# Optimization experiments

Measured on AMD Instinct MI355X. Metric: run time of the kernel, lower is better.

Reference implementation:

```python
import jax, jax.numpy as jnp
import numpy as np
from jax import lax

IN_CH = 512
OUT_CH = 512
K = 3
W_DIM = 512
PAD = K // 2
EPS = 1e-8


def setup_inputs() -> dict:
    key = jax.random.key(0)
    k1, k2, k3, k4 = jax.random.split(key, 4)
    B, H, W = 8, 64, 64
    x = jax.random.normal(k1, (B, IN_CH, H, W), dtype=jnp.float32)
    w = jax.random.normal(k2, (B, W_DIM), dtype=jnp.float32)
    weight = jax.random.normal(k3, (OUT_CH, IN_CH, K, K), dtype=jnp.float32)
    bias = jnp.zeros((OUT_CH,), dtype=jnp.float32)
    # nn.Linear(512, in_ch): weight [in_ch, 512], bias [in_ch]
    lim = 1.0 / np.sqrt(W_DIM)
    affine_w = jax.random.uniform(k4, (IN_CH, W_DIM), dtype=jnp.float32, minval=-lim, maxval=lim)
    affine_b = jnp.zeros((IN_CH,), dtype=jnp.float32)
    return {"x": x, "w": w, "weight": weight, "bias": bias,
            "affine_w": affine_w, "affine_b": affine_b}


def _conv_one(xi, wi):
    # xi: [C, H, W], wi: [O, C, K, K] -> [O, H, W]
    out = lax.conv_general_dilated(
        xi[None], wi, window_strides=(1, 1),
        padding=[(PAD, PAD), (PAD, PAD)],
        dimension_numbers=("NCHW", "OIHW", "NCHW"))
    return out[0]


def reference(x, w, weight, bias, affine_w, affine_b):
    # style: [B, C] -> broadcast as [B, 1, C, 1, 1]
    style = w @ affine_w.T + affine_b
    wmod = weight[None] * (style[:, None, :, None, None] + 1.0)  # [B, O, C, K, K]
    # demodulate
    sigma = lax.rsqrt(jnp.sum(wmod * wmod, axis=(2, 3, 4), keepdims=True) + EPS)
    wmod = wmod * sigma
    # per-sample conv (equivalent to groups=B grouped conv)
    out = jax.vmap(_conv_one)(x, wmod)  # [B, O, H, W]
    return out + bias[None, :, None, None]
```

## Files before the change

### kernel.cpp

```cpp
#include <hip/hip_runtime.h>
#include <hip/hip_bf16.h>

typedef __attribute__((ext_vector_type(8))) short bf16x8;
typedef __attribute__((ext_vector_type(4))) float f32x4;

#define FSW(c) (((c) >> 1) & 3)

static __device__ __forceinline__ uint bf16rne(float f) {
    uint u = __float_as_uint(f);
    return (u + 0x7fffu + ((u >> 16) & 1u)) >> 16;
}

__global__ void k_style(const float* __restrict__ w, const float* __restrict__ aw,
                        const float* __restrict__ ab, float* __restrict__ style) {
    int idx = blockIdx.x * 4 + (threadIdx.x >> 6);
    int lane = threadIdx.x & 63;
    int b = idx >> 9, c = idx & 511;
    const float* wp = w + b * 512;
    const float* ap = aw + (size_t)c * 512;
    float s = 0.f;
    #pragma unroll
    for (int i = 0; i < 8; ++i) s += wp[lane + i * 64] * ap[lane + i * 64];
    #pragma unroll
    for (int m = 32; m; m >>= 1) s += __shfl_xor(s, m, 64);
    if (lane == 0) style[idx] = s + ab[c] + 1.0f;
}

__global__ void k_wprep(const float* __restrict__ weight, ushort* __restrict__ Wf,
                        float* __restrict__ wsq) {
    int t = blockIdx.x * 256 + threadIdx.x;
    int o = t >> 9, c = t & 511;
    int grp = o >> 5, rr = o & 31, fm = rr >> 4, l15r = rr & 15;
    int chunkid = c >> 5, kgw = (c >> 3) & 3, kk = c & 7;
    int lanew = kgw * 16 + l15r;
    const float* wp = weight + (size_t)t * 9;
    size_t G = (size_t)(grp * 16 + chunkid);
    size_t base = G * 9216 + (size_t)fm * 512 + (size_t)lanew * 8 + kk;
    float sq = 0.f;
    #pragma unroll
    for (int j = 0; j < 9; ++j) {
        float v = wp[j];
        sq += v * v;
        Wf[base + (size_t)j * 1024] = (ushort)bf16rne(v);
    }
    wsq[t] = sq;
}

__global__ void k_sigma(const float* __restrict__ style, const float* __restrict__ wsq,
                        float* __restrict__ sigma) {
    int idx = blockIdx.x * 4 + (threadIdx.x >> 6);
    int lane = threadIdx.x & 63;
    int b = idx >> 9, o = idx & 511;
    const float* sp = style + b * 512;
    const float* qp = wsq + (size_t)o * 512;
    float s = 0.f;
    #pragma unroll
    for (int i = 0; i < 8; ++i) {
        float st = sp[lane + i * 64];
        s += st * st * qp[lane + i * 64];
    }
    #pragma unroll
    for (int m = 32; m; m >>= 1) s += __shfl_xor(s, m, 64);
    if (lane == 0) sigma[idx] = rsqrtf(s + 1e-8f);
}

__global__ void k_premod(const float* __restrict__ x, const float* __restrict__ style,
                         ushort* __restrict__ xb) {
    int bid = blockIdx.x;
    int b = bid >> 6, y = bid & 63;
    int xcol = threadIdx.x >> 2, cg = threadIdx.x & 3;
    const float* sp = style + b * 512;
    #pragma unroll 1
    for (int cb = 0; cb < 16; ++cb) {
        int c0 = cb * 32 + cg * 8;
        float v[8];
        #pragma unroll
        for (int j = 0; j < 8; ++j)
            v[j] = x[((size_t)(b * 512 + c0 + j) * 64 + y) * 64 + xcol] * sp[c0 + j];
        uint4 pk;
        pk.x = bf16rne(v[0]) | (bf16rne(v[1]) << 16);
        pk.y = bf16rne(v[2]) | (bf16rne(v[3]) << 16);
        pk.z = bf16rne(v[4]) | (bf16rne(v[5]) << 16);
        pk.w = bf16rne(v[6]) | (bf16rne(v[7]) << 16);
        *(uint4*)&xb[((size_t)(b * 64 + y) * 64 + xcol) * 512 + c0] = pk;
    }
}

#define ALOAD(ARR, G, CC) { \
    const ushort* Wc_ = Wbase + (size_t)(CC) * 9216 + (G) * 3072; \
    _Pragma("unroll") for (int q_ = 0; q_ < 6; ++q_) \
        ARR[q_] = *(const uint4*)(Wc_ + q_ * 512); }

#define MM(AV, BV, FM, FN) \
    acc[FM][FN] = __builtin_amdgcn_mfma_f32_16x16x32_bf16( \
        *(const bf16x8*)&(AV), (BV), acc[FM][FN], 0, 0, 0)

#define HGROUP(AARR, H) \
    _Pragma("unroll") for (int dx_ = 0; dx_ < 3; ++dx_) { \
      _Pragma("unroll") for (int q_ = 0; q_ < 4; ++q_) { \
        MM(AARR[dx_ * 2 + 0], bv[dx_ * 4 + q_], 0, (H) * 4 + q_); \
        MM(AARR[dx_ * 2 + 1], bv[dx_ * 4 + q_], 1, (H) * 4 + q_); \
      } }

#define ROW(R, MFMAS) { \
    bf16x8 bv[12]; \
    _Pragma("unroll") for (int dx_ = 0; dx_ < 3; ++dx_) { \
      _Pragma("unroll") for (int q_ = 0; q_ < 4; ++q_) { \
        int ci_ = dx_ + q_ * 16 + l15; \
        bv[dx_ * 4 + q_] = *(const bf16x8*)&sX[cur][((R) * 66 + ci_) * 32 + ((kg ^ FSW(ci_)) * 8)]; \
      } } \
    __builtin_amdgcn_s_setprio(1); \
    MFMAS \
    __builtin_amdgcn_s_setprio(0); }

__global__ __launch_bounds__(256, 2) void k_conv(
    const ushort* __restrict__ xb, const ushort* __restrict__ Wf,
    const float* __restrict__ sigma, const float* __restrict__ bias,
    float* __restrict__ out) {

    __shared__ ushort sX[2][4 * 66 * 32];

    const int tid = threadIdx.x, bid = blockIdx.x;
    const int ob = bid & 3, pb = bid >> 2;
    const int b = pb >> 5, y0 = (pb & 31) * 2;
    const int o0 = ob * 128;
    const int wv = tid >> 6, lane = tid & 63;
    const int l15 = lane & 15, kg = lane >> 4;

    const int scol = (tid >> 2) & 63;
    const int skg = tid & 3;
    const int colpos = scol + 1;
    const int sslot = (skg ^ FSW(colpos)) * 8;
    const ushort* xrow_base = xb + ((size_t)(b * 64) * 64 + scol) * 512 + skg * 8;

    const int grp = ob * 4 + wv;
    const ushort* Wbase = Wf + (size_t)grp * 147456 + lane * 8;

    f32x4 acc[2][8];
    #pragma unroll
    for (int i = 0; i < 2; ++i)
        #pragma unroll
        for (int j = 0; j < 8; ++j) acc[i][j] = (f32x4){0.f, 0.f, 0.f, 0.f};

    if (tid < 64) {
        int buf = tid >> 5, rem = tid & 31;
        int r = rem >> 3, side = (rem >> 2) & 1, sl = rem & 3;
        int cp = side * 65;
        *(uint4*)&sX[buf][(r * 66 + cp) * 32 + sl * 8] = make_uint4(0u, 0u, 0u, 0u);
    }

    uint4 xs[4];
    #pragma unroll
    for (int p = 0; p < 4; ++p) {
        int yy = y0 - 1 + p;
        xs[p] = ((unsigned)yy < 64u)
              ? *(const uint4*)(xrow_base + (size_t)yy * 32768)
              : make_uint4(0u, 0u, 0u, 0u);
    }
    #pragma unroll
    for (int p = 0; p < 4; ++p)
        *(uint4*)&sX[0][(p * 66 + colpos) * 32 + sslot] = xs[p];

    uint4 a0[6], a1[6], a2[6];
    ALOAD(a0, 0, 0); ALOAD(a1, 1, 0); ALOAD(a2, 2, 0);
    __syncthreads();

    int cur = 0;
    #pragma unroll 1
    for (int cci = 0; cci < 16; ++cci) {
        const int ncc = (cci + 1) & 15;

        #pragma unroll
        for (int p = 0; p < 4; ++p) {
            int yy = y0 - 1 + p;
            xs[p] = ((unsigned)yy < 64u)
                  ? *(const uint4*)(xrow_base + (size_t)yy * 32768 + ncc * 32)
                  : make_uint4(0u, 0u, 0u, 0u);
        }

        ROW(0, HGROUP(a0, 0))
        ROW(1, HGROUP(a0, 1) HGROUP(a1, 0))
        ALOAD(a0, 0, ncc);
        ROW(2, HGROUP(a1, 1) HGROUP(a2, 0))
        ALOAD(a1, 1, ncc);
        ROW(3, HGROUP(a2, 1))
        ALOAD(a2, 2, ncc);

        #pragma unroll
        for (int p = 0; p < 4; ++p)
            *(uint4*)&sX[cur ^ 1][(p * 66 + colpos) * 32 + sslot] = xs[p];
        __syncthreads();
        cur ^= 1;
    }

    const float* sigb = sigma + b * 512;
    #pragma unroll
    for (int fm = 0; fm < 2; ++fm) {
        #pragma unroll
        for (int j = 0; j < 4; ++j) {
            int o = o0 + wv * 32 + fm * 16 + kg * 4 + j;
            float sg = sigb[o];
            float bs = bias[o];
            float* op = out + ((size_t)(b * 512 + o) * 64 + y0) * 64;
            #pragma unroll
            for (int fn = 0; fn < 8; ++fn)
                op[(fn >> 2) * 64 + (fn & 3) * 16 + l15] = acc[fm][fn][j] * sg + bs;
        }
    }
}

extern "C" void kernel_launch(void* const* d_in, const int* in_sizes, int n_in,
                              void* d_out, int out_size, void* d_ws, size_t ws_size,
                              hipStream_t stream) {
    const float* x    = (const float*)d_in[0];
    const float* w    = (const float*)d_in[1];
    const float* wt   = (const float*)d_in[2];
    const float* bias = (const float*)d_in[3];
    const float* aw   = (const float*)d_in[4];
    const float* ab   = (const float*)d_in[5];
    float* out = (float*)d_out;

    float* style  = (float*)d_ws;
    float* sigmap = style + 4096;
    float* wsq    = sigmap + 4096;
    ushort* Wf    = (ushort*)(wsq + 512 * 512);
    ushort* xbm   = Wf + 2359296;

    k_style <<<1024, 256, 0, stream>>>(w, aw, ab, style);
    k_wprep <<<1024, 256, 0, stream>>>(wt, Wf, wsq);
    k_premod<<< 512, 256, 0, stream>>>(x, style, xbm);
    k_sigma <<<1024, 256, 0, stream>>>(style, wsq, sigmap);
    k_conv  <<<1024, 256, 0, stream>>>(xbm, Wf, sigmap, bias, out);
}
```

Before: 150.5 us.

## Switch conv to 32x32x16 MFMA with new weight and LDS layouts

Result: slower. 194.0 us (+28.9%).

```diff
diff --git a/kernel.cpp b/kernel.cpp
--- a/kernel.cpp
+++ b/kernel.cpp
@@ -2,9 +2,7 @@
 #include <hip/hip_bf16.h>
 
 typedef __attribute__((ext_vector_type(8))) short bf16x8;
-typedef __attribute__((ext_vector_type(4))) float f32x4;
-
-#define FSW(c) (((c) >> 1) & 3)
+typedef __attribute__((ext_vector_type(16))) float f32x16;
 
 static __device__ __forceinline__ uint bf16rne(float f) {
     uint u = __float_as_uint(f);
@@ -30,12 +28,12 @@
                         float* __restrict__ wsq) {
     int t = blockIdx.x * 256 + threadIdx.x;
     int o = t >> 9, c = t & 511;
-    int grp = o >> 5, rr = o & 31, fm = rr >> 4, l15r = rr & 15;
-    int chunkid = c >> 5, kgw = (c >> 3) & 3, kk = c & 7;
-    int lanew = kgw * 16 + l15r;
+    int grp = o >> 5, mrow = o & 31;
+    int chunk = c >> 5, ks = (c >> 4) & 1, khi = (c >> 3) & 1, e = c & 7;
+    int lane = khi * 32 + mrow;
+    size_t base = (size_t)(grp * 16 + chunk) * 9216
+                + (size_t)ks * 512 + (size_t)lane * 8 + e;
     const float* wp = weight + (size_t)t * 9;
-    size_t G = (size_t)(grp * 16 + chunkid);
-    size_t base = G * 9216 + (size_t)fm * 512 + (size_t)lanew * 8 + kk;
     float sq = 0.f;
     #pragma unroll
     for (int j = 0; j < 9; ++j) {
@@ -86,31 +84,30 @@
     }
 }
 
-#define ALOAD(ARR, G, CC) { \
-    const ushort* Wc_ = Wbase + (size_t)(CC) * 9216 + (G) * 3072; \
+#define ALOAD(SL, DY, CC) { \
+    const ushort* p_ = Wgrp + (size_t)(CC) * 9216 + (DY) * 3072; \
     _Pragma("unroll") for (int q_ = 0; q_ < 6; ++q_) \
-        ARR[q_] = *(const uint4*)(Wc_ + q_ * 512); }
-
-#define MM(AV, BV, FM, FN) \
-    acc[FM][FN] = __builtin_amdgcn_mfma_f32_16x16x32_bf16( \
-        *(const bf16x8*)&(AV), (BV), acc[FM][FN], 0, 0, 0)
-
-#define HGROUP(AARR, H) \
-    _Pragma("unroll") for (int dx_ = 0; dx_ < 3; ++dx_) { \
-      _Pragma("unroll") for (int q_ = 0; q_ < 4; ++q_) { \
-        MM(AARR[dx_ * 2 + 0], bv[dx_ * 4 + q_], 0, (H) * 4 + q_); \
-        MM(AARR[dx_ * 2 + 1], bv[dx_ * 4 + q_], 1, (H) * 4 + q_); \
-      } }
-
-#define ROW(R, MFMAS) { \
+        SL[q_] = *(const uint4*)(p_ + q_ * 512); }
+
+#define BRD(R, DX, CG, KS) \
+    (*(const bf16x8*)&sX[cur][(((R) * 4 + (KS) * 2 + hi) * 66 + (CG) * 32 + l31 + (DX)) * 8])
+
+#define HG(S, H) \
+    _Pragma("unroll") for (int dx_ = 0; dx_ < 3; ++dx_) \
+    _Pragma("unroll") for (int ks_ = 0; ks_ < 2; ++ks_) \
+    _Pragma("unroll") for (int cg_ = 0; cg_ < 2; ++cg_) \
+        acc[(H) * 2 + cg_] = __builtin_amdgcn_mfma_f32_32x32x16_bf16( \
+            *(const bf16x8*)&S[dx_ * 2 + ks_], bv[dx_ * 4 + cg_ * 2 + ks_], \
+            acc[(H) * 2 + cg_], 0, 0, 0);
+
+#define PHASE(R, BODY) { \
     bf16x8 bv[12]; \
-    _Pragma("unroll") for (int dx_ = 0; dx_ < 3; ++dx_) { \
-      _Pragma("unroll") for (int q_ = 0; q_ < 4; ++q_) { \
-        int ci_ = dx_ + q_ * 16 + l15; \
-        bv[dx_ * 4 + q_] = *(const bf16x8*)&sX[cur][((R) * 66 + ci_) * 32 + ((kg ^ FSW(ci_)) * 8)]; \
-      } } \
+    _Pragma("unroll") for (int dx_ = 0; dx_ < 3; ++dx_) \
+    _Pragma("unroll") for (int cg_ = 0; cg_ < 2; ++cg_) \
+    _Pragma("unroll") for (int ks_ = 0; ks_ < 2; ++ks_) \
+        bv[dx_ * 4 + cg_ * 2 + ks_] = BRD(R, dx_, cg_, ks_); \
     __builtin_amdgcn_s_setprio(1); \
-    MFMAS \
+    BODY \
     __builtin_amdgcn_s_setprio(0); }
 
 __global__ __launch_bounds__(256, 2) void k_conv(
@@ -118,35 +115,31 @@
     const float* __restrict__ sigma, const float* __restrict__ bias,
     float* __restrict__ out) {
 
-    __shared__ ushort sX[2][4 * 66 * 32];
+    __shared__ ushort sX[2][4 * 4 * 66 * 8];
 
     const int tid = threadIdx.x, bid = blockIdx.x;
-    const int ob = bid & 3, pb = bid >> 2;
+    const int pb = bid & 255, ob = bid >> 8;
     const int b = pb >> 5, y0 = (pb & 31) * 2;
-    const int o0 = ob * 128;
     const int wv = tid >> 6, lane = tid & 63;
-    const int l15 = lane & 15, kg = lane >> 4;
-
-    const int scol = (tid >> 2) & 63;
+    const int l31 = lane & 31, hi = lane >> 5;
+
+    const int scol = tid >> 2;
     const int skg = tid & 3;
     const int colpos = scol + 1;
-    const int sslot = (skg ^ FSW(colpos)) * 8;
     const ushort* xrow_base = xb + ((size_t)(b * 64) * 64 + scol) * 512 + skg * 8;
 
     const int grp = ob * 4 + wv;
-    const ushort* Wbase = Wf + (size_t)grp * 147456 + lane * 8;
-
-    f32x4 acc[2][8];
-    #pragma unroll
-    for (int i = 0; i < 2; ++i)
-        #pragma unroll
-        for (int j = 0; j < 8; ++j) acc[i][j] = (f32x4){0.f, 0.f, 0.f, 0.f};
+    const ushort* Wgrp = Wf + (size_t)grp * 147456 + lane * 8;
+
+    f32x16 acc[4];
+    #pragma unroll
+    for (int j = 0; j < 4; ++j)
+        acc[j] = (f32x16){0,0,0,0,0,0,0,0,0,0,0,0,0,0,0,0};
 
     if (tid < 64) {
-        int buf = tid >> 5, rem = tid & 31;
-        int r = rem >> 3, side = (rem >> 2) & 1, sl = rem & 3;
-        int cp = side * 65;
-        *(uint4*)&sX[buf][(r * 66 + cp) * 32 + sl * 8] = make_uint4(0u, 0u, 0u, 0u);
+        int buf = tid >> 5, i = tid & 31;
+        int r = i >> 3, s = (i >> 1) & 3, side = i & 1;
+        *(uint4*)&sX[buf][((r * 4 + s) * 66 + side * 65) * 8] = make_uint4(0u, 0u, 0u, 0u);
     }
 
     uint4 xs[4];
@@ -159,10 +152,10 @@
     }
     #pragma unroll
     for (int p = 0; p < 4; ++p)
-        *(uint4*)&sX[0][(p * 66 + colpos) * 32 + sslot] = xs[p];
+        *(uint4*)&sX[0][((p * 4 + skg) * 66 + colpos) * 8] = xs[p];
 
     uint4 a0[6], a1[6], a2[6];
-    ALOAD(a0, 0, 0); ALOAD(a1, 1, 0); ALOAD(a2, 2, 0);
+    ALOAD(a0, 0, 0) ALOAD(a1, 1, 0) ALOAD(a2, 2, 0)
     __syncthreads();
 
     int cur = 0;
@@ -178,33 +171,33 @@
                   : make_uint4(0u, 0u, 0u, 0u);
         }
 
-        ROW(0, HGROUP(a0, 0))
-        ROW(1, HGROUP(a0, 1) HGROUP(a1, 0))
-        ALOAD(a0, 0, ncc);
-        ROW(2, HGROUP(a1, 1) HGROUP(a2, 0))
-        ALOAD(a1, 1, ncc);
-        ROW(3, HGROUP(a2, 1))
-        ALOAD(a2, 2, ncc);
+        PHASE(0, HG(a0, 0))
+        PHASE(1, HG(a1, 0) HG(a0, 1))
+        ALOAD(a0, 0, ncc)
+        PHASE(2, HG(a2, 0) HG(a1, 1))
+        ALOAD(a1, 1, ncc)
+        PHASE(3, HG(a2, 1))
 
         #pragma unroll
         for (int p = 0; p < 4; ++p)
-            *(uint4*)&sX[cur ^ 1][(p * 66 + colpos) * 32 + sslot] = xs[p];
+            *(uint4*)&sX[cur ^ 1][((p * 4 + skg) * 66 + colpos) * 8] = xs[p];
         __syncthreads();
         cur ^= 1;
+        ALOAD(a2, 2, ncc)
     }
 
     const float* sigb = sigma + b * 512;
     #pragma unroll
-    for (int fm = 0; fm < 2; ++fm) {
-        #pragma unroll
-        for (int j = 0; j < 4; ++j) {
-            int o = o0 + wv * 32 + fm * 16 + kg * 4 + j;
-            float sg = sigb[o];
-            float bs = bias[o];
-            float* op = out + ((size_t)(b * 512 + o) * 64 + y0) * 64;
+    for (int h = 0; h < 2; ++h) {
+        #pragma unroll
+        for (int cg = 0; cg < 2; ++cg) {
             #pragma unroll
-            for (int fn = 0; fn < 8; ++fn)
-                op[(fn >> 2) * 64 + (fn & 3) * 16 + l15] = acc[fm][fn][j] * sg + bs;
+            for (int reg = 0; reg < 16; ++reg) {
+                int row = (reg & 3) + 8 * (reg >> 2) + 4 * hi;
+                int o = grp * 32 + row;
+                float v = acc[h * 2 + cg][reg] * sigb[o] + bias[o];
+                out[(((size_t)(b * 512 + o) * 64) + y0 + h) * 64 + cg * 32 + l31] = v;
+            }
         }
     }
 }
```

## Compute four output rows per conv block to reuse weight fragments

Applied to the files above, without the earlier changes.

Measured after the change: 226.8 us. +50.7%, slower.

```diff
diff --git a/kernel.cpp b/kernel.cpp
--- a/kernel.cpp
+++ b/kernel.cpp
@@ -86,10 +86,10 @@
     }
 }
 
-#define ALOAD(ARR, G, CC) { \
-    const ushort* Wc_ = Wbase + (size_t)(CC) * 9216 + (G) * 3072; \
+#define ALOAD(SL, DY, CC) { \
+    const ushort* p_ = Wbase + (size_t)(CC) * 9216 + (DY) * 3072; \
     _Pragma("unroll") for (int q_ = 0; q_ < 6; ++q_) \
-        ARR[q_] = *(const uint4*)(Wc_ + q_ * 512); }
+        SL[q_] = *(const uint4*)(p_ + q_ * 512); }
 
 #define MM(AV, BV, FM, FN) \
     acc[FM][FN] = __builtin_amdgcn_mfma_f32_16x16x32_bf16( \
@@ -104,11 +104,11 @@
 
 #define ROW(R, MFMAS) { \
     bf16x8 bv[12]; \
-    _Pragma("unroll") for (int dx_ = 0; dx_ < 3; ++dx_) { \
-      _Pragma("unroll") for (int q_ = 0; q_ < 4; ++q_) { \
+    _Pragma("unroll") for (int dx_ = 0; dx_ < 3; ++dx_) \
+    _Pragma("unroll") for (int q_ = 0; q_ < 4; ++q_) { \
         int ci_ = dx_ + q_ * 16 + l15; \
         bv[dx_ * 4 + q_] = *(const bf16x8*)&sX[cur][((R) * 66 + ci_) * 32 + ((kg ^ FSW(ci_)) * 8)]; \
-      } } \
+    } \
     __builtin_amdgcn_s_setprio(1); \
     MFMAS \
     __builtin_amdgcn_s_setprio(0); }
@@ -118,11 +118,11 @@
     const float* __restrict__ sigma, const float* __restrict__ bias,
     float* __restrict__ out) {
 
-    __shared__ ushort sX[2][4 * 66 * 32];
+    __shared__ ushort sX[2][6 * 66 * 32];
 
     const int tid = threadIdx.x, bid = blockIdx.x;
     const int ob = bid & 3, pb = bid >> 2;
-    const int b = pb >> 5, y0 = (pb & 31) * 2;
+    const int b = pb >> 4, y0 = (pb & 15) * 4;
     const int o0 = ob * 128;
     const int wv = tid >> 6, lane = tid & 63;
     const int l15 = lane & 15, kg = lane >> 4;
@@ -136,33 +136,32 @@
     const int grp = ob * 4 + wv;
     const ushort* Wbase = Wf + (size_t)grp * 147456 + lane * 8;
 
-    f32x4 acc[2][8];
+    f32x4 acc[2][16];
     #pragma unroll
     for (int i = 0; i < 2; ++i)
         #pragma unroll
-        for (int j = 0; j < 8; ++j) acc[i][j] = (f32x4){0.f, 0.f, 0.f, 0.f};
-
-    if (tid < 64) {
-        int buf = tid >> 5, rem = tid & 31;
-        int r = rem >> 3, side = (rem >> 2) & 1, sl = rem & 3;
-        int cp = side * 65;
-        *(uint4*)&sX[buf][(r * 66 + cp) * 32 + sl * 8] = make_uint4(0u, 0u, 0u, 0u);
-    }
-
-    uint4 xs[4];
-    #pragma unroll
-    for (int p = 0; p < 4; ++p) {
+        for (int j = 0; j < 16; ++j) acc[i][j] = (f32x4){0.f, 0.f, 0.f, 0.f};
+
+    if (tid < 96) {
+        int buf = tid >= 48, i = tid % 48;
+        int r = i >> 3, side = (i >> 2) & 1, sl = i & 3;
+        *(uint4*)&sX[buf][(r * 66 + side * 65) * 32 + sl * 8] = make_uint4(0u, 0u, 0u, 0u);
+    }
+
+    uint4 xs[6];
+    #pragma unroll
+    for (int p = 0; p < 6; ++p) {
         int yy = y0 - 1 + p;
         xs[p] = ((unsigned)yy < 64u)
               ? *(const uint4*)(xrow_base + (size_t)yy * 32768)
               : make_uint4(0u, 0u, 0u, 0u);
     }
     #pragma unroll
-    for (int p = 0; p < 4; ++p)
+    for (int p = 0; p < 6; ++p)
         *(uint4*)&sX[0][(p * 66 + colpos) * 32 + sslot] = xs[p];
 
     uint4 a0[6], a1[6], a2[6];
-    ALOAD(a0, 0, 0); ALOAD(a1, 1, 0); ALOAD(a2, 2, 0);
+    ALOAD(a0, 0, 0) ALOAD(a1, 1, 0) ALOAD(a2, 2, 0)
     __syncthreads();
 
     int cur = 0;
@@ -171,7 +170,7 @@
         const int ncc = (cci + 1) & 15;
 
         #pragma unroll
-        for (int p = 0; p < 4; ++p) {
+        for (int p = 0; p < 6; ++p) {
             int yy = y0 - 1 + p;
             xs[p] = ((unsigned)yy < 64u)
                   ? *(const uint4*)(xrow_base + (size_t)yy * 32768 + ncc * 32)
@@ -180,17 +179,21 @@
 
         ROW(0, HGROUP(a0, 0))
         ROW(1, HGROUP(a0, 1) HGROUP(a1, 0))
-        ALOAD(a0, 0, ncc);
-        ROW(2, HGROUP(a1, 1) HGROUP(a2, 0))
-        ALOAD(a1, 1, ncc);
-        ROW(3, HGROUP(a2, 1))
-        ALOAD(a2, 2, ncc);
-
-        #pragma unroll
-        for (int p = 0; p < 4; ++p)
+
+        #pragma unroll
+        for (int p = 0; p < 6; ++p)
             *(uint4*)&sX[cur ^ 1][(p * 66 + colpos) * 32 + sslot] = xs[p];
+
+        ROW(2, HGROUP(a0, 2) HGROUP(a1, 1) HGROUP(a2, 0))
+        ROW(3, HGROUP(a0, 3) HGROUP(a1, 2) HGROUP(a2, 1))
+        ALOAD(a0, 0, ncc)
+        ROW(4, HGROUP(a1, 3) HGROUP(a2, 2))
+        ALOAD(a1, 1, ncc)
+        ROW(5, HGROUP(a2, 3))
+
         __syncthreads();
         cur ^= 1;
+        ALOAD(a2, 2, ncc)
     }
 
     const float* sigb = sigma + b * 512;
@@ -203,8 +206,10 @@
             float bs = bias[o];
             float* op = out + ((size_t)(b * 512 + o) * 64 + y0) * 64;
             #pragma unroll
-            for (int fn = 0; fn < 8; ++fn)
-                op[(fn >> 2) * 64 + (fn & 3) * 16 + l15] = acc[fm][fn][j] * sg + bs;
+            for (int h = 0; h < 4; ++h)
+                #pragma unroll
+                for (int q = 0; q < 4; ++q)
+                    op[h * 64 + q * 16 + l15] = acc[fm][h * 4 + q][j] * sg + bs;
         }
     }
 }
@@ -230,5 +235,5 @@
     k_wprep <<<1024, 256, 0, stream>>>(wt, Wf, wsq);
     k_premod<<< 512, 256, 0, stream>>>(x, style, xbm);
     k_sigma <<<1024, 256, 0, stream>>>(style, wsq, sigmap);
-    k_conv  <<<1024, 256, 0, stream>>>(xbm, Wf, sigmap, bias, out);
-}
+    k_conv  <<< 512, 256, 0, stream>>>(xbm, Wf, sigmap, bias, out);
+}
```

## Cut conv weight register buffers from three to two for higher occupancy

Applied to the files above, without the earlier changes.

New measurement: 330.5 us. +119.6%, slower.

```diff
diff --git a/kernel.cpp b/kernel.cpp
--- a/kernel.cpp
+++ b/kernel.cpp
@@ -86,10 +86,10 @@
     }
 }
 
-#define ALOAD(ARR, G, CC) { \
-    const ushort* Wc_ = Wbase + (size_t)(CC) * 9216 + (G) * 3072; \
+#define ALOAD(SL, DY, CC) { \
+    const ushort* p_ = Wbase + (size_t)(CC) * 9216 + (DY) * 3072; \
     _Pragma("unroll") for (int q_ = 0; q_ < 6; ++q_) \
-        ARR[q_] = *(const uint4*)(Wc_ + q_ * 512); }
+        SL[q_] = *(const uint4*)(p_ + q_ * 512); }
 
 #define MM(AV, BV, FM, FN) \
     acc[FM][FN] = __builtin_amdgcn_mfma_f32_16x16x32_bf16( \
@@ -104,16 +104,40 @@
 
 #define ROW(R, MFMAS) { \
     bf16x8 bv[12]; \
-    _Pragma("unroll") for (int dx_ = 0; dx_ < 3; ++dx_) { \
-      _Pragma("unroll") for (int q_ = 0; q_ < 4; ++q_) { \
+    _Pragma("unroll") for (int dx_ = 0; dx_ < 3; ++dx_) \
+    _Pragma("unroll") for (int q_ = 0; q_ < 4; ++q_) { \
         int ci_ = dx_ + q_ * 16 + l15; \
         bv[dx_ * 4 + q_] = *(const bf16x8*)&sX[cur][((R) * 66 + ci_) * 32 + ((kg ^ FSW(ci_)) * 8)]; \
-      } } \
+    } \
     __builtin_amdgcn_s_setprio(1); \
     MFMAS \
     __builtin_amdgcn_s_setprio(0); }
 
-__global__ __launch_bounds__(256, 2) void k_conv(
+#define CHUNK(CCI, NCC, A0_, A1_) { \
+     \
+    _Pragma("unroll") \
+    for (int p = 0; p < 4; ++p) { \
+        int yy = y0 - 1 + p; \
+        xs[p] = ((unsigned)yy < 64u) \
+              ? *(const uint4*)(xrow_base + (size_t)yy * 32768 + (NCC) * 32) \
+              : make_uint4(0u, 0u, 0u, 0u); \
+    } \
+    ROW(0, HGROUP(A0_, 0)) \
+    ROW(1, HGROUP(A0_, 1) HGROUP(A1_, 0)) \
+    ALOAD(A0_, 2, CCI)             \
+     \
+    _Pragma("unroll") \
+    for (int p = 0; p < 4; ++p) \
+        *(uint4*)&sX[cur ^ 1][(p * 66 + colpos) * 32 + sslot] = xs[p]; \
+    ROW(2, HGROUP(A1_, 1) HGROUP(A0_, 0)) \
+    ALOAD(A1_, 0, NCC)             \
+    ROW(3, HGROUP(A0_, 1)) \
+    ALOAD(A0_, 1, NCC)             \
+    __syncthreads(); \
+    cur ^= 1; \
+}
+
+__global__ __launch_bounds__(256, 3) void k_conv(
     const ushort* __restrict__ xb, const ushort* __restrict__ Wf,
     const float* __restrict__ sigma, const float* __restrict__ bias,
     float* __restrict__ out) {
@@ -161,36 +185,16 @@
     for (int p = 0; p < 4; ++p)
         *(uint4*)&sX[0][(p * 66 + colpos) * 32 + sslot] = xs[p];
 
-    uint4 a0[6], a1[6], a2[6];
-    ALOAD(a0, 0, 0); ALOAD(a1, 1, 0); ALOAD(a2, 2, 0);
+    uint4 aX[6], aY[6];
+    ALOAD(aX, 0, 0) ALOAD(aY, 1, 0)
     __syncthreads();
 
     int cur = 0;
     #pragma unroll 1
-    for (int cci = 0; cci < 16; ++cci) {
-        const int ncc = (cci + 1) & 15;
-
-        #pragma unroll
-        for (int p = 0; p < 4; ++p) {
-            int yy = y0 - 1 + p;
-            xs[p] = ((unsigned)yy < 64u)
-                  ? *(const uint4*)(xrow_base + (size_t)yy * 32768 + ncc * 32)
-                  : make_uint4(0u, 0u, 0u, 0u);
-        }
-
-        ROW(0, HGROUP(a0, 0))
-        ROW(1, HGROUP(a0, 1) HGROUP(a1, 0))
-        ALOAD(a0, 0, ncc);
-        ROW(2, HGROUP(a1, 1) HGROUP(a2, 0))
-        ALOAD(a1, 1, ncc);
-        ROW(3, HGROUP(a2, 1))
-        ALOAD(a2, 2, ncc);
-
-        #pragma unroll
-        for (int p = 0; p < 4; ++p)
-            *(uint4*)&sX[cur ^ 1][(p * 66 + colpos) * 32 + sslot] = xs[p];
-        __syncthreads();
-        cur ^= 1;
+    for (int it = 0; it < 8; ++it) {
+        const int c0i = it * 2, c1i = c0i + 1, c2i = (c0i + 2) & 15;
+        CHUNK(c0i, c1i, aX, aY)
+        CHUNK(c1i, c2i, aY, aX)
     }
 
     const float* sigb = sigma + b * 512;
```
